# Kernel tuning notes

Hardware: AMD Instinct MI355X
Metric: run time of the kernel (lower is better)

The kernel has to match this reference:

```python
import jax, jax.numpy as jnp
import numpy as np
import math

B, L, D, H = 4, 2048, 1024, 16
DK = D // H


def setup_inputs() -> dict:
    key = jax.random.key(0)
    ks = jax.random.split(key, 12)
    scale = math.sqrt(6.0 / (D + D))  # xavier_uniform for square Linear
    def lin(k):
        return jax.random.uniform(k, (D, D), jnp.float32, -scale, scale)
    inp = {
        "query": jax.random.normal(ks[0], (B, L, D), jnp.float32),
        "key": jax.random.normal(ks[1], (B, L, D), jnp.float32),
        "value": jax.random.normal(ks[2], (B, L, D), jnp.float32),
        "Wq": lin(ks[3]), "bq": jnp.zeros((D,), jnp.float32),
        "Wk": lin(ks[4]), "bk": jnp.zeros((D,), jnp.float32),
        "Wv": lin(ks[5]), "bv": jnp.zeros((D,), jnp.float32),
        "Wo": lin(ks[6]), "bo": jnp.zeros((D,), jnp.float32),
        # causal mask: True means masked (hide future positions)
        "attn_mask": jnp.triu(jnp.ones((L, L), dtype=bool), k=1),
    }
    return inp


def reference(query, key, value, Wq, bq, Wk, bk, Wv, bv, Wo, bo, attn_mask):
    def proj(x, W, b):
        # torch Linear: x @ W.T + b ; then split heads -> [B, H, L, DK]
        y = jnp.einsum('bld,ed->ble', x, W) + b
        return y.reshape(B, L, H, DK).transpose(0, 2, 1, 3)

    q = proj(query, Wq, bq)
    k = proj(key, Wk, bk)
    v = proj(value, Wv, bv)

    scores = jnp.einsum('bhqd,bhkd->bhqk', q, k) / jnp.sqrt(jnp.float32(DK))
    scores = jnp.where(attn_mask[None, None, :, :], jnp.float32(-jnp.inf), scores)
    p_attn = jax.nn.softmax(scores, axis=-1)  # dropout p=0 (eval)

    ctx = jnp.einsum('bhqk,bhkd->bhqd', p_attn, v)
    ctx = ctx.transpose(0, 2, 1, 3).reshape(B, L, D)
    out = jnp.einsum('bld,ed->ble', ctx, Wo) + bo
    return out
```

## Files before the change

kernel.cpp:

```cpp
#include <hip/hip_runtime.h>
#include <hip/hip_bf16.h>
#include <stdint.h>

typedef unsigned short u16;
typedef unsigned int u32;
typedef short short8 __attribute__((ext_vector_type(8)));
typedef float f32x4 __attribute__((ext_vector_type(4)));
typedef float f32x16 __attribute__((ext_vector_type(16)));
typedef u32 u32x4 __attribute__((ext_vector_type(4)));
typedef u32 u32x2 __attribute__((ext_vector_type(2)));

#define DEV static __device__ __forceinline__

constexpr int Bsz = 4, Lseq = 2048, Dm = 1024, Hn = 16, Dk = 64;
constexpr float LOG2E = 1.44269504088896340736f;
constexpr float QSCALE = 0.125f * LOG2E;

DEV u16 f2bf(float x) {
    u32 u = __builtin_bit_cast(u32, x);
    return (u16)((u + 0x7fffu + ((u >> 16) & 1u)) >> 16);
}

DEV u32 pk2(float a, float b) {
    __hip_bfloat162 h = __float22bfloat162_rn(float2{a, b});
    u32 r;
    __builtin_memcpy(&r, &h, 4);
    return r;
}

DEV u32x4 ld8_cvt(const float* p) {
    f32x4 lo = *(const f32x4*)p;
    f32x4 hi = *(const f32x4*)(p + 4);
    u32x4 r;
    r[0] = pk2(lo[0], lo[1]);
    r[1] = pk2(lo[2], lo[3]);
    r[2] = pk2(hi[0], hi[1]);
    r[3] = pk2(hi[2], hi[3]);
    return r;
}

DEV void glds16(const void* g, void* l) {
    __builtin_amdgcn_global_load_lds(
        (const __attribute__((address_space(1))) void*)g,
        (__attribute__((address_space(3))) void*)l, 16, 0, 0);
}

DEV void pswap(u32& a, u32& b) {
    asm volatile("v_permlane32_swap_b32 %0, %1" : "+v"(a), "+v"(b));
}

DEV short8 mk8(u32 w0, u32 w1, u32 w2, u32 w3) {
    u32x4 t;
    t[0] = w0; t[1] = w1; t[2] = w2; t[3] = w3;
    short8 r;
    __builtin_memcpy(&r, &t, 16);
    return r;
}

__global__ __launch_bounds__(256) void cvt_w3(
    const float* __restrict__ a, const float* __restrict__ b,
    const float* __restrict__ c, u16* __restrict__ d, int n8)
{
    int i = blockIdx.x * 256 + threadIdx.x;
    if (i >= n8) return;
    const float* s = blockIdx.y == 0 ? a : (blockIdx.y == 1 ? b : c);
    ((u32x4*)(d + (size_t)blockIdx.y * (size_t)n8 * 8))[i] = ld8_cvt(s + (long)i * 8);
}

__global__ __launch_bounds__(256) void gemm_oproj(
    const u16* __restrict__ A, const float* __restrict__ W,
    const float* __restrict__ bias, float* __restrict__ Cout)
{
    __shared__ u16 At[2][128 * 32];
    __shared__ u16 Bt[2][128 * 32];

    const int tid = threadIdx.x;
    const int lane = tid & 63, wid = tid >> 6;
    const int wr = wid >> 1, wc = wid & 1;
    const int mbase = blockIdx.x * 128, nbase = blockIdx.y * 128;

    f32x4 acc[4][4];
#pragma unroll
    for (int i = 0; i < 4; i++)
#pragma unroll
        for (int j = 0; j < 4; j++) acc[i][j] = (f32x4)0.f;

    const int srow = lane >> 2;
    const int sseg = (lane & 3) * 8;
    auto stageA = [&](int kt, int buf) {
#pragma unroll
        for (int c = 0; c < 2; c++) {
            const int sec = wid * 2 + c;
            glds16(A + (long)(mbase + sec * 16 + srow) * Dm + (long)kt * 32 + sseg,
                   &At[buf][sec * 512]);
        }
    };

    u32x4 vb[2];
    auto loadB = [&](int kt) {
#pragma unroll
        for (int i = 0; i < 2; i++) {
            int idx = i * 256 + tid;
            int row = idx >> 2, seg = idx & 3;
            vb[i] = ld8_cvt(W + (long)(nbase + row) * Dm + (long)kt * 32 + seg * 8);
        }
    };
    auto writeB = [&](int buf) {
#pragma unroll
        for (int i = 0; i < 2; i++) {
            int idx = i * 256 + tid;
            *(u32x4*)&Bt[buf][idx * 8] = vb[i];
        }
    };

    stageA(0, 0);
    loadB(0);
    writeB(0);
    __syncthreads();

    for (int kt = 0; kt < 32; kt++) {
        const int cur = kt & 1;
        const bool more = (kt + 1 < 32);
        if (more) {
            stageA(kt + 1, cur ^ 1);
            loadB(kt + 1);
        }
        short8 af[4], bfr[4];
#pragma unroll
        for (int mf = 0; mf < 4; mf++)
            af[mf] = *(const short8*)&At[cur][(wr * 64 + mf * 16 + (lane & 15)) * 32 + (lane >> 4) * 8];
#pragma unroll
        for (int nf = 0; nf < 4; nf++)
            bfr[nf] = *(const short8*)&Bt[cur][(wc * 64 + nf * 16 + (lane & 15)) * 32 + (lane >> 4) * 8];
        __builtin_amdgcn_s_setprio(1);
#pragma unroll
        for (int mf = 0; mf < 4; mf++)
#pragma unroll
            for (int nf = 0; nf < 4; nf++)
                acc[mf][nf] = __builtin_amdgcn_mfma_f32_16x16x32_bf16(af[mf], bfr[nf], acc[mf][nf], 0, 0, 0);
        __builtin_amdgcn_s_setprio(0);
        if (more) writeB(cur ^ 1);
        __syncthreads();
    }

#pragma unroll
    for (int nf = 0; nf < 4; nf++) {
        const int n = nbase + wc * 64 + nf * 16 + (lane & 15);
        const float bv = bias[n];
#pragma unroll
        for (int mf = 0; mf < 4; mf++) {
            const int m0 = mbase + wr * 64 + mf * 16 + (lane >> 4) * 4;
#pragma unroll
            for (int r = 0; r < 4; r++) {
                const int m = m0 + r;
                Cout[(long)m * Dm + n] = acc[mf][nf][r] + bv;
            }
        }
    }
}

__global__ __launch_bounds__(256) void gemm_qkv(
    const float* __restrict__ Xq, const float* __restrict__ Xk,
    const float* __restrict__ Xv, const u16* __restrict__ Wb3,
    const float* __restrict__ bq, const float* __restrict__ bk,
    const float* __restrict__ bv, u16* __restrict__ Out3)
{
    __shared__ u16 At[2][128 * 32];
    __shared__ u16 Bt[2][128 * 32];

    const int tid = threadIdx.x;
    const int lane = tid & 63, wid = tid >> 6;
    const int wr = wid >> 1, wc = wid & 1;
    const int mbase = blockIdx.x * 128;
    const int t = blockIdx.y >> 3;
    const int nbase = (blockIdx.y & 7) * 128;
    const float* X = t == 0 ? Xq : (t == 1 ? Xk : Xv);
    const u16* Bw = Wb3 + (size_t)t * Dm * Dm;
    const float* bias = t == 0 ? bq : (t == 1 ? bk : bv);
    const float scale = t == 0 ? QSCALE : 1.0f;
    u16* Cout = Out3 + (size_t)t * ((size_t)Bsz * Lseq * Dm);

    f32x4 acc[4][4];
#pragma unroll
    for (int i = 0; i < 4; i++)
#pragma unroll
        for (int j = 0; j < 4; j++) acc[i][j] = (f32x4)0.f;

    const int srow = lane >> 2;
    const int sseg = (lane & 3) * 8;
    auto stageB = [&](int kt, int buf) {
#pragma unroll
        for (int c = 0; c < 2; c++) {
            const int sec = wid * 2 + c;
            glds16(Bw + (long)(nbase + sec * 16 + srow) * Dm + (long)kt * 32 + sseg,
                   &Bt[buf][sec * 512]);
        }
    };

    u32x4 va[2];
    auto loadA = [&](int kt) {
#pragma unroll
        for (int i = 0; i < 2; i++) {
            int idx = i * 256 + tid;
            int row = idx >> 2, seg = idx & 3;
            va[i] = ld8_cvt(X + (long)(mbase + row) * Dm + (long)kt * 32 + seg * 8);
        }
    };
    auto writeA = [&](int buf) {
#pragma unroll
        for (int i = 0; i < 2; i++) {
            int idx = i * 256 + tid;
            *(u32x4*)&At[buf][idx * 8] = va[i];
        }
    };

    stageB(0, 0);
    loadA(0);
    writeA(0);
    __syncthreads();

    for (int kt = 0; kt < 32; kt++) {
        const int cur = kt & 1;
        const bool more = (kt + 1 < 32);
        if (more) {
            stageB(kt + 1, cur ^ 1);
            loadA(kt + 1);
        }
        short8 af[4], bfr[4];
#pragma unroll
        for (int mf = 0; mf < 4; mf++)
            af[mf] = *(const short8*)&At[cur][(wr * 64 + mf * 16 + (lane & 15)) * 32 + (lane >> 4) * 8];
#pragma unroll
        for (int nf = 0; nf < 4; nf++)
            bfr[nf] = *(const short8*)&Bt[cur][(wc * 64 + nf * 16 + (lane & 15)) * 32 + (lane >> 4) * 8];
        __builtin_amdgcn_s_setprio(1);
#pragma unroll
        for (int mf = 0; mf < 4; mf++)
#pragma unroll
            for (int nf = 0; nf < 4; nf++)
                acc[mf][nf] = __builtin_amdgcn_mfma_f32_16x16x32_bf16(af[mf], bfr[nf], acc[mf][nf], 0, 0, 0);
        __builtin_amdgcn_s_setprio(0);
        if (more) writeA(cur ^ 1);
        __syncthreads();
    }

#pragma unroll
    for (int nf = 0; nf < 4; nf++) {
        const int n = nbase + wc * 64 + nf * 16 + (lane & 15);
        const float bv = bias[n];
#pragma unroll
        for (int mf = 0; mf < 4; mf++) {
            const int m0 = mbase + wr * 64 + mf * 16 + (lane >> 4) * 4;
#pragma unroll
            for (int r = 0; r < 4; r++) {
                const int m = m0 + r;
                const float v = (acc[mf][nf][r] + bv) * scale;
                int b = m >> 11, l = m & 2047, h = n >> 6, dk = n & 63;
                long addr = ((long)(b * Hn + h) * Lseq + l) * Dk + dk;
                Cout[addr] = f2bf(v);
            }
        }
    }
}

__global__ __launch_bounds__(256) void attn_fwd(
    const u16* __restrict__ Qb, const u16* __restrict__ Kb,
    const u16* __restrict__ Vb, u16* __restrict__ Ctx)
{
    __shared__ u16 Kt[2][64 * 64];
    __shared__ u16 Vt[2][64 * 64];

    const int tid = threadIdx.x, lane = tid & 63, w = tid >> 6;
    const int qt = gridDim.y - 1 - blockIdx.y;
    const int bh = blockIdx.x;
    const long base = (long)bh * Lseq * Dk;
    const int qw = qt * 128 + w * 32;
    const int qcol = lane & 31, hi = lane >> 5;

    const int krow_in_w = lane >> 3;
    const int kseg = lane & 7;
    const int vp = tid >> 3;
    const int vd0 = (tid & 7) * 8;

    auto stage_k = [&](int kvbase, int buf) {
#pragma unroll
        for (int c = 0; c < 2; c++) {
            int kv = w * 16 + c * 8 + krow_in_w;
            int d0 = ((kseg ^ (kv & 7)) * 8);
            glds16(Kb + base + (long)(kvbase + kv) * Dk + d0,
                   &Kt[buf][(w * 16 + c * 8) * 64]);
        }
    };

    auto write_v = [&](int buf, const u32x4& r0, const u32x4& r1) {
        const u16* p0 = (const u16*)&r0;
        const u16* p1 = (const u16*)&r1;
#pragma unroll
        for (int j = 0; j < 8; j++) {
            int d = vd0 + j;
            u32 pr = (u32)p0[j] | ((u32)p1[j] << 16);
            int kvx = (2 * vp) ^ ((((d & 7) ^ (d >> 3)) & 7) << 3);
            *(u32*)&Vt[buf][d * 64 + kvx] = pr;
        }
    };

    short8 qfr[4];
#pragma unroll
    for (int ks = 0; ks < 4; ks++)
        qfr[ks] = *(const short8*)(Qb + base + (long)(qw + qcol) * Dk + ks * 16 + hi * 8);

    f32x16 acc0 = (f32x16)0.f, acc1 = (f32x16)0.f;
    float m_run = -__builtin_inff();
    float l_part = 0.f;

    u32x4 vr0, vr1;
    stage_k(0, 0);
    vr0 = *(const u32x4*)(Vb + base + (long)(2 * vp) * Dk + vd0);
    vr1 = *(const u32x4*)(Vb + base + (long)(2 * vp + 1) * Dk + vd0);
    write_v(0, vr0, vr1);
    __syncthreads();

    const int nkv = qt * 2 + 2;
    const int myn = ((qw + 31) >> 6) + 1;

    for (int kvt = 0; kvt < nkv; kvt++) {
        const int cur = kvt & 1;
        const bool more = (kvt + 1 < nkv);
        const int kvbase = kvt * 64;

        if (more) {
            stage_k(kvbase + 64, cur ^ 1);
            vr0 = *(const u32x4*)(Vb + base + (long)(kvbase + 64 + 2 * vp) * Dk + vd0);
            vr1 = *(const u32x4*)(Vb + base + (long)(kvbase + 64 + 2 * vp + 1) * Dk + vd0);
        }

        if (kvt < myn) {
            f32x16 st0 = (f32x16)0.f, st1 = (f32x16)0.f;
            __builtin_amdgcn_s_setprio(1);
#pragma unroll
            for (int ks = 0; ks < 4; ks++) {
                const int d0 = ks * 16 + hi * 8;
                {
                    const int kvrow = qcol;
                    short8 kf = *(const short8*)&Kt[cur][kvrow * 64 + (d0 ^ ((kvrow & 7) << 3))];
                    st0 = __builtin_amdgcn_mfma_f32_32x32x16_bf16(kf, qfr[ks], st0, 0, 0, 0);
                }
                {
                    const int kvrow = 32 + qcol;
                    short8 kf = *(const short8*)&Kt[cur][kvrow * 64 + (d0 ^ ((kvrow & 7) << 3))];
                    st1 = __builtin_amdgcn_mfma_f32_32x32x16_bf16(kf, qfr[ks], st1, 0, 0, 0);
                }
            }
            __builtin_amdgcn_s_setprio(0);

            if ((kvbase + 63) > qw) {
                const int q = qw + qcol;
#pragma unroll
                for (int r = 0; r < 16; r++) {
                    const int rr = (r & 3) + 8 * (r >> 2) + 4 * hi;
                    if (kvbase + rr > q) st0[r] = -1e30f;
                    if (kvbase + 32 + rr > q) st1[r] = -1e30f;
                }
            }

            float tmax = st0[0];
#pragma unroll
            for (int r = 1; r < 16; r++) tmax = fmaxf(tmax, st0[r]);
#pragma unroll
            for (int r = 0; r < 16; r++) tmax = fmaxf(tmax, st1[r]);
            tmax = fmaxf(tmax, __shfl_xor(tmax, 32, 64));
            const bool norescale = __all((int)(tmax <= m_run + 8.f));
            if (!norescale) {
                const float mnew = fmaxf(m_run, tmax);
                const float sc = __builtin_exp2f(m_run - mnew);
                m_run = mnew;
                l_part *= sc;
#pragma unroll
                for (int r = 0; r < 16; r++) {
                    acc0[r] *= sc;
                    acc1[r] *= sc;
                }
            }
            float ts = 0.f;
#pragma unroll
            for (int r = 0; r < 16; r++) {
                float p = __builtin_exp2f(st0[r] - m_run);
                st0[r] = p;
                ts += p;
            }
#pragma unroll
            for (int r = 0; r < 16; r++) {
                float p = __builtin_exp2f(st1[r] - m_run);
                st1[r] = p;
                ts += p;
            }
            l_part += ts;

            short8 pf[4];
            {
                u32 a0 = pk2(st0[0], st0[1]), a1 = pk2(st0[2], st0[3]);
                u32 b0 = pk2(st0[4], st0[5]), b1 = pk2(st0[6], st0[7]);
                pswap(a0, b0);
                pswap(a1, b1);
                pf[0] = mk8(a0, a1, b0, b1);
                u32 c0 = pk2(st0[8], st0[9]), c1 = pk2(st0[10], st0[11]);
                u32 e0 = pk2(st0[12], st0[13]), e1 = pk2(st0[14], st0[15]);
                pswap(c0, e0);
                pswap(c1, e1);
                pf[1] = mk8(c0, c1, e0, e1);
            }
            {
                u32 a0 = pk2(st1[0], st1[1]), a1 = pk2(st1[2], st1[3]);
                u32 b0 = pk2(st1[4], st1[5]), b1 = pk2(st1[6], st1[7]);
                pswap(a0, b0);
                pswap(a1, b1);
                pf[2] = mk8(a0, a1, b0, b1);
                u32 c0 = pk2(st1[8], st1[9]), c1 = pk2(st1[10], st1[11]);
                u32 e0 = pk2(st1[12], st1[13]), e1 = pk2(st1[14], st1[15]);
                pswap(c0, e0);
                pswap(c1, e1);
                pf[3] = mk8(c0, c1, e0, e1);
            }

            __builtin_amdgcn_s_setprio(1);
#pragma unroll
            for (int s = 0; s < 4; s++) {
                {
                    const int d = qcol;
                    const int kvi = (s * 16 + hi * 8) ^ ((((d & 7) ^ (d >> 3)) & 7) << 3);
                    short8 vf = *(const short8*)&Vt[cur][d * 64 + kvi];
                    acc0 = __builtin_amdgcn_mfma_f32_32x32x16_bf16(vf, pf[s], acc0, 0, 0, 0);
                }
                {
                    const int d = 32 + qcol;
                    const int kvi = (s * 16 + hi * 8) ^ ((((d & 7) ^ (d >> 3)) & 7) << 3);
                    short8 vf = *(const short8*)&Vt[cur][d * 64 + kvi];
                    acc1 = __builtin_amdgcn_mfma_f32_32x32x16_bf16(vf, pf[s], acc1, 0, 0, 0);
                }
            }
            __builtin_amdgcn_s_setprio(0);
        }

        if (more) write_v(cur ^ 1, vr0, vr1);
        __syncthreads();
    }

    const int b = bh >> 4, hh = bh & 15;
    float l = l_part + __shfl_xor(l_part, 32, 64);
    const float inv = 1.f / l;
    const int q = qw + qcol;
    const long rowaddr = ((long)b * Lseq + q) * Dm + hh * Dk;
#pragma unroll
    for (int quad = 0; quad < 4; quad++) {
        {
            const int dk0 = quad * 8 + 4 * hi;
            u32x2 o;
            o[0] = pk2(acc0[quad * 4 + 0] * inv, acc0[quad * 4 + 1] * inv);
            o[1] = pk2(acc0[quad * 4 + 2] * inv, acc0[quad * 4 + 3] * inv);
            *(u32x2*)(Ctx + rowaddr + dk0) = o;
        }
        {
            const int dk0 = 32 + quad * 8 + 4 * hi;
            u32x2 o;
            o[0] = pk2(acc1[quad * 4 + 0] * inv, acc1[quad * 4 + 1] * inv);
            o[1] = pk2(acc1[quad * 4 + 2] * inv, acc1[quad * 4 + 3] * inv);
            *(u32x2*)(Ctx + rowaddr + dk0) = o;
        }
    }
}

extern "C" void kernel_launch(void* const* d_in, const int* in_sizes, int n_in,
                              void* d_out, int out_size, void* d_ws, size_t ws_size,
                              hipStream_t stream)
{
    const float* query = (const float*)d_in[0];
    const float* key_  = (const float*)d_in[1];
    const float* value = (const float*)d_in[2];
    const float* Wq = (const float*)d_in[3];
    const float* bq = (const float*)d_in[4];
    const float* Wk = (const float*)d_in[5];
    const float* bk = (const float*)d_in[6];
    const float* Wv = (const float*)d_in[7];
    const float* bv = (const float*)d_in[8];
    const float* Wo = (const float*)d_in[9];
    const float* bo = (const float*)d_in[10];

    float* out = (float*)d_out;
    const size_t tens = (size_t)Bsz * Lseq * Dm;
    const size_t wTot = (size_t)Dm * Dm;
    u16* Qb = (u16*)d_ws;
    u16* Kb = Qb + tens;
    u16* Vb = Kb + tens;
    u16* Cx = Vb + tens;
    u16* Wqb = Cx;

    dim3 blk(256), g(64, 8), gq(64, 24);
    const int n8w = (int)(wTot / 8);
    const int gw = (n8w + 255) / 256;

    cvt_w3<<<dim3(gw, 3), blk, 0, stream>>>(Wq, Wk, Wv, Wqb, n8w);
    gemm_qkv<<<gq, blk, 0, stream>>>(query, key_, value, Wqb, bq, bk, bv, Qb);
    attn_fwd<<<dim3(Bsz * Hn, Lseq / 128), blk, 0, stream>>>(Qb, Kb, Vb, Cx);
    gemm_oproj<<<g, blk, 0, stream>>>(Cx, Wo, bo, out);
}
```

Measured before the change: 210.1 us.

## Split attention KV tile into two 32-row halves with per-half online softmax

```diff
diff --git a/kernel.cpp b/kernel.cpp
--- a/kernel.cpp
+++ b/kernel.cpp
@@ -55,6 +55,24 @@
     short8 r;
     __builtin_memcpy(&r, &t, 16);
     return r;
+}
+
+DEV float max16(const f32x16& v) {
+    float a0 = fmaxf(v[0], v[1]),   a1 = fmaxf(v[2], v[3]);
+    float a2 = fmaxf(v[4], v[5]),   a3 = fmaxf(v[6], v[7]);
+    float a4 = fmaxf(v[8], v[9]),   a5 = fmaxf(v[10], v[11]);
+    float a6 = fmaxf(v[12], v[13]), a7 = fmaxf(v[14], v[15]);
+    float b0 = fmaxf(a0, a1), b1 = fmaxf(a2, a3);
+    float b2 = fmaxf(a4, a5), b3 = fmaxf(a6, a7);
+    return fmaxf(fmaxf(b0, b1), fmaxf(b2, b3));
+}
+DEV float sum16(const f32x16& v) {
+    float a0 = v[0] + v[1],   a1 = v[2] + v[3];
+    float a2 = v[4] + v[5],   a3 = v[6] + v[7];
+    float a4 = v[8] + v[9],   a5 = v[10] + v[11];
+    float a6 = v[12] + v[13], a7 = v[14] + v[15];
+    float b0 = a0 + a1, b1 = a2 + a3, b2 = a4 + a5, b3 = a6 + a7;
+    return (b0 + b1) + (b2 + b3);
 }
 
 __global__ __launch_bounds__(256) void cvt_w3(
@@ -263,7 +281,7 @@
     }
 }
 
-__global__ __launch_bounds__(256) void attn_fwd(
+__global__ __launch_bounds__(256, 4) void attn_fwd(
     const u16* __restrict__ Qb, const u16* __restrict__ Kb,
     const u16* __restrict__ Vb, u16* __restrict__ Ctx)
 {
@@ -335,110 +353,81 @@
         }
 
         if (kvt < myn) {
-            f32x16 st0 = (f32x16)0.f, st1 = (f32x16)0.f;
-            __builtin_amdgcn_s_setprio(1);
-#pragma unroll
-            for (int ks = 0; ks < 4; ks++) {
-                const int d0 = ks * 16 + hi * 8;
+            const bool need_mask = (kvbase + 63) > qw;
+#pragma unroll
+            for (int hf = 0; hf < 2; hf++) {
+                f32x16 st = (f32x16)0.f;
+                __builtin_amdgcn_s_setprio(1);
+#pragma unroll
+                for (int ks = 0; ks < 4; ks++) {
+                    const int d0 = ks * 16 + hi * 8;
+                    const int kvrow = hf * 32 + qcol;
+                    short8 kf = *(const short8*)&Kt[cur][kvrow * 64 + (d0 ^ ((kvrow & 7) << 3))];
+                    st = __builtin_amdgcn_mfma_f32_32x32x16_bf16(kf, qfr[ks], st, 0, 0, 0);
+                }
+                __builtin_amdgcn_s_setprio(0);
+
+                if (need_mask) {
+                    const int q = qw + qcol;
+#pragma unroll
+                    for (int r = 0; r < 16; r++) {
+                        const int rr = (r & 3) + 8 * (r >> 2) + 4 * hi + hf * 32;
+                        if (kvbase + rr > q) st[r] = -1e30f;
+                    }
+                }
+
+                float tmax = max16(st);
+                tmax = fmaxf(tmax, __shfl_xor(tmax, 32, 64));
+                const bool norescale = __all((int)(tmax <= m_run + 8.f));
+                if (!norescale) {
+                    const float mnew = fmaxf(m_run, tmax);
+                    const float sc = __builtin_exp2f(m_run - mnew);
+                    m_run = mnew;
+                    l_part *= sc;
+#pragma unroll
+                    for (int r = 0; r < 16; r++) {
+                        acc0[r] *= sc;
+                        acc1[r] *= sc;
+                    }
+                }
+#pragma unroll
+                for (int r = 0; r < 16; r++) st[r] = __builtin_exp2f(st[r] - m_run);
+                l_part += sum16(st);
+
+                short8 pf0, pf1;
                 {
-                    const int kvrow = qcol;
-                    short8 kf = *(const short8*)&Kt[cur][kvrow * 64 + (d0 ^ ((kvrow & 7) << 3))];
-                    st0 = __builtin_amdgcn_mfma_f32_32x32x16_bf16(kf, qfr[ks], st0, 0, 0, 0);
+                    u32 a0 = pk2(st[0], st[1]), a1 = pk2(st[2], st[3]);
+                    u32 b0 = pk2(st[4], st[5]), b1 = pk2(st[6], st[7]);
+                    pswap(a0, b0);
+                    pswap(a1, b1);
+                    pf0 = mk8(a0, a1, b0, b1);
+                    u32 c0 = pk2(st[8], st[9]), c1 = pk2(st[10], st[11]);
+                    u32 e0 = pk2(st[12], st[13]), e1 = pk2(st[14], st[15]);
+                    pswap(c0, e0);
+                    pswap(c1, e1);
+                    pf1 = mk8(c0, c1, e0, e1);
                 }
-                {
-                    const int kvrow = 32 + qcol;
-                    short8 kf = *(const short8*)&Kt[cur][kvrow * 64 + (d0 ^ ((kvrow & 7) << 3))];
-                    st1 = __builtin_amdgcn_mfma_f32_32x32x16_bf16(kf, qfr[ks], st1, 0, 0, 0);
+
+                __builtin_amdgcn_s_setprio(1);
+#pragma unroll
+                for (int s = 0; s < 2; s++) {
+                    const short8 pf = s == 0 ? pf0 : pf1;
+                    const int kvs = (hf * 2 + s) * 16 + hi * 8;
+                    {
+                        const int d = qcol;
+                        const int kvi = kvs ^ ((((d & 7) ^ (d >> 3)) & 7) << 3);
+                        short8 vf = *(const short8*)&Vt[cur][d * 64 + kvi];
+                        acc0 = __builtin_amdgcn_mfma_f32_32x32x16_bf16(vf, pf, acc0, 0, 0, 0);
+                    }
+                    {
+                        const int d = 32 + qcol;
+                        const int kvi = kvs ^ ((((d & 7) ^ (d >> 3)) & 7) << 3);
+                        short8 vf = *(const short8*)&Vt[cur][d * 64 + kvi];
+                        acc1 = __builtin_amdgcn_mfma_f32_32x32x16_bf16(vf, pf, acc1, 0, 0, 0);
+                    }
                 }
+                __builtin_amdgcn_s_setprio(0);
             }
-            __builtin_amdgcn_s_setprio(0);
-
-            if ((kvbase + 63) > qw) {
-                const int q = qw + qcol;
-#pragma unroll
-                for (int r = 0; r < 16; r++) {
-                    const int rr = (r & 3) + 8 * (r >> 2) + 4 * hi;
-                    if (kvbase + rr > q) st0[r] = -1e30f;
-                    if (kvbase + 32 + rr > q) st1[r] = -1e30f;
-                }
-            }
-
-            float tmax = st0[0];
-#pragma unroll
-            for (int r = 1; r < 16; r++) tmax = fmaxf(tmax, st0[r]);
-#pragma unroll
-            for (int r = 0; r < 16; r++) tmax = fmaxf(tmax, st1[r]);
-            tmax = fmaxf(tmax, __shfl_xor(tmax, 32, 64));
-            const bool norescale = __all((int)(tmax <= m_run + 8.f));
-            if (!norescale) {
-                const float mnew = fmaxf(m_run, tmax);
-                const float sc = __builtin_exp2f(m_run - mnew);
-                m_run = mnew;
-                l_part *= sc;
-#pragma unroll
-                for (int r = 0; r < 16; r++) {
-                    acc0[r] *= sc;
-                    acc1[r] *= sc;
-                }
-            }
-            float ts = 0.f;
-#pragma unroll
-            for (int r = 0; r < 16; r++) {
-                float p = __builtin_exp2f(st0[r] - m_run);
-                st0[r] = p;
-                ts += p;
-            }
-#pragma unroll
-            for (int r = 0; r < 16; r++) {
-                float p = __builtin_exp2f(st1[r] - m_run);
-                st1[r] = p;
-                ts += p;
-            }
-            l_part += ts;
-
-            short8 pf[4];
-            {
-                u32 a0 = pk2(st0[0], st0[1]), a1 = pk2(st0[2], st0[3]);
-                u32 b0 = pk2(st0[4], st0[5]), b1 = pk2(st0[6], st0[7]);
-                pswap(a0, b0);
-                pswap(a1, b1);
-                pf[0] = mk8(a0, a1, b0, b1);
-                u32 c0 = pk2(st0[8], st0[9]), c1 = pk2(st0[10], st0[11]);
-                u32 e0 = pk2(st0[12], st0[13]), e1 = pk2(st0[14], st0[15]);
-                pswap(c0, e0);
-                pswap(c1, e1);
-                pf[1] = mk8(c0, c1, e0, e1);
-            }
-            {
-                u32 a0 = pk2(st1[0], st1[1]), a1 = pk2(st1[2], st1[3]);
-                u32 b0 = pk2(st1[4], st1[5]), b1 = pk2(st1[6], st1[7]);
-                pswap(a0, b0);
-                pswap(a1, b1);
-                pf[2] = mk8(a0, a1, b0, b1);
-                u32 c0 = pk2(st1[8], st1[9]), c1 = pk2(st1[10], st1[11]);
-                u32 e0 = pk2(st1[12], st1[13]), e1 = pk2(st1[14], st1[15]);
-                pswap(c0, e0);
-                pswap(c1, e1);
-                pf[3] = mk8(c0, c1, e0, e1);
-            }
-
-            __builtin_amdgcn_s_setprio(1);
-#pragma unroll
-            for (int s = 0; s < 4; s++) {
-                {
-                    const int d = qcol;
-                    const int kvi = (s * 16 + hi * 8) ^ ((((d & 7) ^ (d >> 3)) & 7) << 3);
-                    short8 vf = *(const short8*)&Vt[cur][d * 64 + kvi];
-                    acc0 = __builtin_amdgcn_mfma_f32_32x32x16_bf16(vf, pf[s], acc0, 0, 0, 0);
-                }
-                {
-                    const int d = 32 + qcol;
-                    const int kvi = (s * 16 + hi * 8) ^ ((((d & 7) ^ (d >> 3)) & 7) << 3);
-                    short8 vf = *(const short8*)&Vt[cur][d * 64 + kvi];
-                    acc1 = __builtin_amdgcn_mfma_f32_32x32x16_bf16(vf, pf[s], acc1, 0, 0, 0);
-                }
-            }
-            __builtin_amdgcn_s_setprio(0);
         }
 
         if (more) write_v(cur ^ 1, vr0, vr1);
```

After: 212.6 us. Within noise of the previous version (+1.2%).
